# Performance work log

Measured on AMD Instinct MI355X. Metric: run time of the kernel, lower is better.

## Reference

```python
import jax, jax.numpy as jnp
import numpy as np

KS = 2        # kernel_size
DIL = 1       # dilation
FILTERS = 512
Z_DIM = 128
B, C, T = 8, 512, 4096
TZ = T + 2 * (KS - 1)


def _conv1d(x, w, b):
    # x: (B, L, Cin), w: (ks, Cin, Cout) -> VALID conv, channels-last (keras Conv1D)
    y = jax.lax.conv_general_dilated(x, w, window_strides=(1,), padding='VALID',
                                     dimension_numbers=('NWC', 'WIO', 'NWC'))
    return y + b


def _adaptor(z, w1, b1, w2, b2):
    return _conv1d(jax.nn.relu(_conv1d(z, w1, b1)), w2, b2)


def setup_inputs() -> dict:
    key = jax.random.key(0)
    ks = jax.random.split(key, 10)
    lim = np.sqrt(6.0 / FILTERS)
    u = lambda k, shp: jax.random.uniform(k, shp, jnp.float32, -lim, lim)
    return {
        'x': jax.random.normal(ks[0], (B, C, T), jnp.float32),
        'z': jax.random.normal(ks[1], (B, TZ, Z_DIM), jnp.float32),
        'ww1': u(ks[2], (KS, Z_DIM, FILTERS)), 'wb1': jnp.zeros((FILTERS,), jnp.float32),
        'ww2': u(ks[3], (KS, FILTERS, FILTERS)), 'wb2': jnp.zeros((FILTERS,), jnp.float32),
        'bw1': u(ks[4], (KS, Z_DIM, FILTERS)), 'bb1': jnp.zeros((FILTERS,), jnp.float32),
        'bw2': u(ks[5], (KS, FILTERS, FILTERS)), 'bb2': jnp.zeros((FILTERS,), jnp.float32),
    }


def reference(x, z, ww1, wb1, ww2, wb2, bw1, bb1, bw2, bb2):
    m = x.shape[1]
    t = x.shape[2]
    pad = DIL * (KS - 1)
    xp = jnp.pad(x, ((0, 0), (0, 0), (0, pad)))
    end = t + pad
    # im2col-style unfold: (B, C*KS, T)
    xu = jnp.concatenate([xp[:, :, pad - i * DIL: end - i * DIL] for i in range(KS)], axis=1)
    weights = _adaptor(z, ww1, wb1, ww2, wb2)   # (B, T, F)
    bias = _adaptor(z, bw1, bb1, bw2, bb2)      # (B, T, F)
    y = jnp.matmul(xu, weights)                 # (B, C*KS, F)
    return y[:, :m, :] + bias[:, :m, :]
```

## Files before the change

### kernel.cpp

```cpp
#include <hip/hip_runtime.h>

typedef short short8 __attribute__((ext_vector_type(8)));
typedef float float4v __attribute__((ext_vector_type(4)));
typedef __attribute__((address_space(1))) const unsigned int gu32;
typedef __attribute__((address_space(3))) unsigned int lu32;

__device__ __forceinline__ unsigned short f2bf(float f) {
  unsigned int u = __builtin_bit_cast(unsigned int, f);
  u += 0x7FFFu + ((u >> 16) & 1u);
  return (unsigned short)(u >> 16);
}
__device__ __forceinline__ float bf2f(unsigned short s) {
  return __builtin_bit_cast(float, (unsigned int)s << 16);
}

template<int N> __device__ __forceinline__ void vmwait() {
  if constexpr (N == 0) asm volatile("s_waitcnt vmcnt(0)" ::: "memory");
  else if constexpr (N == 2) asm volatile("s_waitcnt vmcnt(2)" ::: "memory");
  else if constexpr (N == 3) asm volatile("s_waitcnt vmcnt(3)" ::: "memory");
  else if constexpr (N == 4) asm volatile("s_waitcnt vmcnt(4)" ::: "memory");
  else if constexpr (N == 6) asm volatile("s_waitcnt vmcnt(6)" ::: "memory");
  else if constexpr (N == 8) asm volatile("s_waitcnt vmcnt(8)" ::: "memory");
}

__global__ __launch_bounds__(256) void prep_w(
    const float* __restrict__ ww1, const float* __restrict__ ww2,
    const float* __restrict__ bw1, const float* __restrict__ bw2,
    const float* __restrict__ z,
    unsigned short* __restrict__ w1T, unsigned short* __restrict__ w2T,
    unsigned short* __restrict__ b1T, unsigned short* __restrict__ b2T,
    unsigned short* __restrict__ zb)
{
  int i = blockIdx.x * 256 + threadIdx.x;
  if (i < 131072) {
    int n = i & 511, k = i >> 9;
    w1T[n * 256 + k] = f2bf(ww1[i]);
  } else if (i < 655360) {
    int j = i - 131072; int n = j & 511, k = j >> 9;
    w2T[n * 1024 + k] = f2bf(ww2[j]);
  } else if (i < 786432) {
    int j = i - 655360; int n = j & 511, k = j >> 9;
    b1T[n * 256 + k] = f2bf(bw1[j]);
  } else if (i < 1310720) {
    int j = i - 786432; int n = j & 511, k = j >> 9;
    b2T[n * 1024 + k] = f2bf(bw2[j]);
  } else {
    int j = i - 1310720;
    zb[j] = f2bf(z[j]);
  }
}

template<int BM, int BN, bool RELU, bool OBF16, bool TRANS, bool SPLITK, int NH,
         bool ROWPACK, bool DBUF>
__device__ __forceinline__ void gemm_core(
    int bx, int by, int bz, int nzTot, unsigned short* smem,
    const unsigned short* __restrict__ A,
    const unsigned short* __restrict__ A2,
    const unsigned short* __restrict__ Bt,
    const float* __restrict__ biasv,
    void* __restrict__ outp,
    void* __restrict__ outp2,
    int M, int Kchunk, int RPB, int EXTRA, int BSCALE,
    int nHalf, int bRowMask,
    long long bStrideB, long long outBatchStride, int outLd)
{
  constexpr int WM = BM / 2, WN = BN / 2;
  constexpr int NI = WM / 16, NJ = WN / 16;
  constexpr int AI = BM / 64;
  constexpr int BI = BN / 64;
  constexpr int SA1 = BM * 32, SB1 = BN * 32;
  unsigned short* sB0 = smem + NH * SA1;

  const int tid  = threadIdx.x;
  const int lane = tid & 63;
  const int wave = tid >> 6;
  const int wm = wave >> 1, wn = wave & 1;
  const int lr = lane & 15, quad = lane >> 4;

  const int r0 = bx * BM;
  const int n0 = by * BN;
  const int bb = r0 / RPB;
  const int Ktot = SPLITK ? Kchunk * nzTot : Kchunk;
  const int kOff = SPLITK ? bz * Kchunk : 0;
  const long long bOffB = (long long)bb * bStrideB;
  const unsigned short* Ae = (nHalf && n0 >= nHalf) ? A2 : A;

  const int srow = lane >> 2;
  const int sg = (lane & 3) ^ (srow & 3);
  const unsigned short* gA[AI];
#pragma unroll
  for (int c = 0; c < AI; ++c) {
    int instr = c * 4 + wave;
    int row = instr * 16 + srow;
    int r = r0 + row; if (r > M - 1) r = M - 1;
    gA[c] = Ae + ((long long)r + (long long)(r / RPB) * EXTRA) * BSCALE + kOff + sg * 8;
  }
  const unsigned short* gB[BI];
#pragma unroll
  for (int c = 0; c < BI; ++c) {
    int instr = c * 4 + wave;
    int row = instr * 16 + srow;
    gB[c] = Bt + (long long)((n0 + row) & bRowMask) * Ktot + bOffB + kOff + sg * 8;
  }

  int aoff[NI], boff[NJ];
#pragma unroll
  for (int i = 0; i < NI; ++i) {
    int rr = wm * WM + i * 16 + lr;
    aoff[i] = rr * 32 + ((quad ^ (rr & 3)) * 8);
  }
#pragma unroll
  for (int j = 0; j < NJ; ++j) {
    int rr = wn * WN + j * 16 + lr;
    boff[j] = rr * 32 + ((quad ^ (rr & 3)) * 8);
  }

  float4v acc[NI][NJ];
  const float4v z4 = {0.f, 0.f, 0.f, 0.f};
#pragma unroll
  for (int i = 0; i < NI; ++i)
#pragma unroll
    for (int j = 0; j < NJ; ++j) acc[i][j] = z4;

  if (DBUF) {
    constexpr int RS = SA1 + SB1;
    const int NT = Kchunk >> 5;
    auto stg = [&](int t, int m) {
      unsigned short* rb = smem + m * RS;
      int kk = t * 32;
#pragma unroll
      for (int c = 0; c < AI; ++c)
        __builtin_amdgcn_global_load_lds((gu32*)(gA[c] + kk),
                                         (lu32*)(rb + (c * 4 + wave) * 512), 16, 0, 0);
#pragma unroll
      for (int c = 0; c < BI; ++c)
        __builtin_amdgcn_global_load_lds((gu32*)(gB[c] + kk),
                                         (lu32*)(rb + SA1 + (c * 4 + wave) * 512), 16, 0, 0);
    };
    stg(0, 0); stg(1, 1);
    int m = 0;
    for (int t = 0; t < NT; ++t) {
      if (t + 1 < NT) vmwait<AI + BI>();
      else            vmwait<0>();
      __builtin_amdgcn_s_barrier();
      __builtin_amdgcn_sched_barrier(0);
      int m2 = m + 2; if (m2 >= 3) m2 -= 3;
      if (t + 2 < NT) stg(t + 2, m2);
      const unsigned short* rb = smem + m * RS;
      short8 af[NI], bfr[NJ];
#pragma unroll
      for (int i = 0; i < NI; ++i) af[i] = *(const short8*)(rb + aoff[i]);
#pragma unroll
      for (int j = 0; j < NJ; ++j) bfr[j] = *(const short8*)(rb + SA1 + boff[j]);
#pragma unroll
      for (int i = 0; i < NI; ++i)
#pragma unroll
        for (int j = 0; j < NJ; ++j)
          acc[i][j] = __builtin_amdgcn_mfma_f32_16x16x32_bf16(af[i], bfr[j], acc[i][j], 0, 0, 0);
      if (++m == 3) m = 0;
    }
    __syncthreads();
  } else {
    for (int k0 = 0; k0 < Kchunk; k0 += 32 * NH) {
#pragma unroll
      for (int h = 0; h < NH; ++h) {
#pragma unroll
        for (int c = 0; c < AI; ++c)
          __builtin_amdgcn_global_load_lds((gu32*)(gA[c] + k0 + h * 32),
                                           (lu32*)(smem + (c * 4 + wave) * 512 + h * SA1), 16, 0, 0);
#pragma unroll
        for (int c = 0; c < BI; ++c)
          __builtin_amdgcn_global_load_lds((gu32*)(gB[c] + k0 + h * 32),
                                           (lu32*)(sB0 + (c * 4 + wave) * 512 + h * SB1), 16, 0, 0);
      }
      __syncthreads();
#pragma unroll
      for (int h = 0; h < NH; ++h) {
        short8 af[NI], bfr[NJ];
#pragma unroll
        for (int i = 0; i < NI; ++i) af[i] = *(const short8*)(smem + h * SA1 + aoff[i]);
#pragma unroll
        for (int j = 0; j < NJ; ++j) bfr[j] = *(const short8*)(sB0 + h * SB1 + boff[j]);
#pragma unroll
        for (int i = 0; i < NI; ++i)
#pragma unroll
          for (int j = 0; j < NJ; ++j)
            acc[i][j] = __builtin_amdgcn_mfma_f32_16x16x32_bf16(af[i], bfr[j], acc[i][j], 0, 0, 0);
      }
      __syncthreads();
    }
  }

  if (TRANS) {
    unsigned short* Ts = smem;
    const int t0l = r0 - bb * RPB;
#pragma unroll
    for (int p = 0; p < 2; ++p) {
      if (wn == p) {
#pragma unroll
        for (int j = 0; j < NJ; ++j) {
          int frl = j * 16 + lr;
          float bv = biasv[n0 + p * WN + frl];
#pragma unroll
          for (int i = 0; i < NI; ++i) {
            int tr = wm * WM + i * 16 + quad * 4;
            unsigned long long pk = 0;
#pragma unroll
            for (int g = 0; g < 4; ++g) {
              float vv = acc[i][j][g] + bv;
              if (RELU) vv = fmaxf(vv, 0.f);
              pk |= (unsigned long long)f2bf(vv) << (16 * g);
            }
            *(unsigned long long*)(Ts + frl * (BM + 8) + tr) = pk;
          }
        }
      }
      __syncthreads();
      int frl = tid >> 2, sgg = tid & 3;
      unsigned short* dst = (unsigned short*)outp + (long long)bb * outBatchStride
                          + (long long)(n0 + p * WN + frl) * outLd + t0l + sgg * (BM / 4);
      const unsigned short* srcp = Ts + frl * (BM + 8) + sgg * (BM / 4);
#pragma unroll
      for (int u = 0; u < BM / 32; ++u)
        *(uint4*)(dst + u * 8) = *(const uint4*)(srcp + u * 8);
      __syncthreads();
    }
  } else if (ROWPACK) {
    constexpr int P  = (BM > 64) ? 2 : 1;
    constexpr int RP = BM / P;
    constexpr int BNP = BN + 8;
    constexpr int TPR = 256 / RP;
    constexpr int EPT = BN / TPR;
    void* op = (SPLITK && bz) ? outp2 : outp;
    unsigned short* R = smem;
#pragma unroll
    for (int p = 0; p < P; ++p) {
      if (P == 1 || wm == p) {
#pragma unroll
        for (int j = 0; j < NJ; ++j) {
          int cc = wn * WN + j * 16 + lr;
#pragma unroll
          for (int i = 0; i < NI; ++i) {
            int rl = (P == 1 ? wm * WM : 0) + i * 16 + quad * 4;
#pragma unroll
            for (int g = 0; g < 4; ++g)
              R[(rl + g) * BNP + cc] = f2bf(acc[i][j][g]);
          }
        }
      }
      __syncthreads();
      int rloc = tid / TPR, part = tid % TPR;
      unsigned short* dstp = (unsigned short*)op
                           + (long long)(r0 + p * RP + rloc) * outLd + n0 + part * EPT;
      const unsigned short* srcp = R + rloc * BNP + part * EPT;
#pragma unroll
      for (int u = 0; u < EPT / 8; ++u)
        *(uint4*)(dstp + u * 8) = *(const uint4*)(srcp + u * 8);
      if (p + 1 < P) __syncthreads();
    }
  } else {
    void* op = (SPLITK && bz) ? outp2 : outp;
#pragma unroll
    for (int j = 0; j < NJ; ++j) {
      int n_g = n0 + wn * WN + j * 16 + lr;
      float bv = biasv ? biasv[n_g] : 0.f;
#pragma unroll
      for (int i = 0; i < NI; ++i) {
        int r_base = r0 + wm * WM + i * 16 + quad * 4;
#pragma unroll
        for (int g = 0; g < 4; ++g) {
          int r_g = r_base + g;
          if (r_g >= M) continue;
          float v = acc[i][j][g] + bv;
          if (RELU) v = fmaxf(v, 0.f);
          long long oidx = (long long)r_g * outLd + n_g;
          if (OBF16) ((unsigned short*)op)[oidx] = f2bf(v);
          else       ((float*)op)[oidx] = v;
        }
      }
    }
  }
}

template<int BM, int BN, bool RELU, bool OBF16, bool TRANS, bool SPLITK, int NH,
         bool ROWPACK, bool DBUF, bool REMAP8>
__global__ __launch_bounds__(256)
void gemm_bt(const unsigned short* __restrict__ A,
             const unsigned short* __restrict__ A2,
             const unsigned short* __restrict__ Bt,
             const float* __restrict__ biasv,
             void* __restrict__ outp,
             void* __restrict__ outp2,
             int M, int Kchunk, int RPB, int EXTRA, int BSCALE,
             int nHalf, int bRowMask,
             long long bStrideB, long long outBatchStride, int outLd)
{
  constexpr int STAGE = DBUF ? 3 * (BM * 32 + BN * 32) : NH * (BM * 32 + BN * 32);
  constexpr int REPK = TRANS ? (BN / 2) * (BM + 8)
                     : (ROWPACK ? (BM > 64 ? (BM / 2) * (BN + 8) : BM * (BN + 8)) : 0);
  constexpr int SMEMN = (REPK > STAGE) ? REPK : STAGE;
  __shared__ unsigned short smem[SMEMN];
  int bx, by, bz, nz;
  if (REMAP8) {
    int lin = blockIdx.x;
    by = lin & 7;
    int pos = lin >> 3;
    bz = pos >> 5;
    bx = pos & 31;
    nz = 2;
  } else {
    bx = blockIdx.x; by = blockIdx.y; bz = blockIdx.z; nz = gridDim.z;
  }
  gemm_core<BM, BN, RELU, OBF16, TRANS, SPLITK, NH, ROWPACK, DBUF>(
      bx, by, bz, nz, smem,
      A, A2, Bt, biasv, outp, outp2,
      M, Kchunk, RPB, EXTRA, BSCALE, nHalf, bRowMask,
      bStrideB, outBatchStride, outLd);
}

__global__ __launch_bounds__(256) void cvt_x(
    const float* __restrict__ x,
    unsigned short* __restrict__ xs,
    unsigned short* __restrict__ xz,
    float* __restrict__ rs)
{
  __shared__ float red[4];
  long long r = blockIdx.x;
  const float* xr = x + r * 4096;
  int t0 = threadIdx.x * 16;
  float v[17];
  const float4* xr4 = (const float4*)(xr + t0);
#pragma unroll
  for (int q = 0; q < 4; ++q) {
    float4 f = xr4[q];
    v[q * 4] = f.x; v[q * 4 + 1] = f.y; v[q * 4 + 2] = f.z; v[q * 4 + 3] = f.w;
  }
  v[16] = (t0 + 16 < 4096) ? xr[t0 + 16] : 0.f;
  unsigned int spk[8], zpk[8];
  float sum = 0.f;
#pragma unroll
  for (int q = 0; q < 8; ++q) {
    unsigned short s0 = f2bf(v[2 * q + 1]);
    unsigned short s1 = f2bf(v[2 * q + 2]);
    sum += bf2f(s0);
    sum += bf2f(s1);
    spk[q] = (unsigned int)s0 | ((unsigned int)s1 << 16);
    unsigned short z0 = (t0 == 0 && q == 0) ? (unsigned short)0 : f2bf(v[2 * q]);
    unsigned short z1 = f2bf(v[2 * q + 1]);
    zpk[q] = (unsigned int)z0 | ((unsigned int)z1 << 16);
  }
  *(uint4*)(xs + r * 4096 + t0)     = *(uint4*)(spk);
  *(uint4*)(xs + r * 4096 + t0 + 8) = *(uint4*)(spk + 4);
  *(uint4*)(xz + r * 4096 + t0)     = *(uint4*)(zpk);
  *(uint4*)(xz + r * 4096 + t0 + 8) = *(uint4*)(zpk + 4);
#pragma unroll
  for (int off = 32; off > 0; off >>= 1) sum += __shfl_down(sum, off);
  if ((threadIdx.x & 63) == 0) red[threadIdx.x >> 6] = sum;
  __syncthreads();
  if (threadIdx.x == 0) rs[r] = red[0] + red[1] + red[2] + red[3];
}

__global__ __launch_bounds__(256) void conv1(
    const unsigned short* __restrict__ zb,
    const unsigned short* __restrict__ w1T,
    const unsigned short* __restrict__ b1T,
    const float* __restrict__ wb1,
    const float* __restrict__ bb1,
    unsigned short* __restrict__ h1T,
    unsigned short* __restrict__ h1b)
{
  __shared__ unsigned short smem[24576];
  int g = blockIdx.x;
  if (g < 1024) {
    gemm_core<128, 128, true, true, true, false, 1, false, true>(
        g & 255, g >> 8, 0, 1, smem,
        zb, nullptr, w1T, wb1, h1T, nullptr,
        32768, 256, 4096, 2, 128, 0, 0xFFFF, 0, 512ll * 4096, 4096);
  } else {
    int idx = g - 1024;
    gemm_core<64, 128, true, true, false, false, 1, false, true>(
        idx % 65, idx / 65, 0, 1, smem,
        zb, nullptr, b1T, bb1, h1b, nullptr,
        4104, 256, 513, 3585, 128, 0, 0xFFFF, 0, 0, 512);
  }
}

__global__ __launch_bounds__(256) void final_gemm3(
    const unsigned short* __restrict__ p0,
    const unsigned short* __restrict__ p1,
    const unsigned short* __restrict__ h1b,
    const unsigned short* __restrict__ w2T,
    const unsigned short* __restrict__ b2T,
    const float* __restrict__ rs,
    const float* __restrict__ wb2,
    const float* __restrict__ bb2,
    float* __restrict__ out)
{
  constexpr int RS = 8192;
  __shared__ unsigned short smem[3 * RS];
  const int tid = threadIdx.x;
  const int lane = tid & 63, wave = tid >> 6;
  const int wm = wave >> 1, wn = wave & 1;
  const int lr = lane & 15, quad = lane >> 4;
  const int r0 = blockIdx.x * 64, n0 = blockIdx.y * 64;

  const int srow = lane >> 2;
  const int sg = (lane & 3) ^ (srow & 3);
  const int row = wave * 16 + srow;
  const int rA = r0 + row;
  const int rB = n0 + row;
  const unsigned short* aP[3] = {
    p0 + (long long)rA * 1024 + sg * 8,
    p1 + (long long)rA * 1024 + sg * 8,
    h1b + ((long long)rA + (rA >> 9)) * 512 + sg * 8 };
  const unsigned short* bP[3] = {
    w2T + (long long)rB * 1024 + sg * 8,
    w2T + (long long)rB * 1024 + sg * 8,
    b2T + (long long)rB * 1024 + sg * 8 };

  int aoff[2], boff[2];
#pragma unroll
  for (int i = 0; i < 2; ++i) {
    int rr = wm * 32 + i * 16 + lr;
    aoff[i] = rr * 32 + ((quad ^ (rr & 3)) * 8);
    int nn = wn * 32 + i * 16 + lr;
    boff[i] = nn * 32 + ((quad ^ (nn & 3)) * 8);
  }

  float4v acc[2][2];
  const float4v z4 = {0.f, 0.f, 0.f, 0.f};
  acc[0][0] = z4; acc[0][1] = z4; acc[1][0] = z4; acc[1][1] = z4;

  const int wslot = wave * 512;
  auto stg = [&](int t, int m) {
    int k = t * 64; int seg = k >> 10; int kk = k & 1023;
    unsigned short* base = smem + m * RS;
    __builtin_amdgcn_global_load_lds((gu32*)(aP[seg] + kk),      (lu32*)(base + wslot), 16, 0, 0);
    __builtin_amdgcn_global_load_lds((gu32*)(aP[seg] + kk + 32), (lu32*)(base + 2048 + wslot), 16, 0, 0);
    __builtin_amdgcn_global_load_lds((gu32*)(bP[seg] + kk),      (lu32*)(base + 4096 + wslot), 16, 0, 0);
    __builtin_amdgcn_global_load_lds((gu32*)(bP[seg] + kk + 32), (lu32*)(base + 6144 + wslot), 16, 0, 0);
  };
  stg(0, 0); stg(1, 1);
  int m = 0;
  for (int t = 0; t < 48; ++t) {
    if (t < 47) vmwait<4>();
    else        vmwait<0>();
    __builtin_amdgcn_s_barrier();
    __builtin_amdgcn_sched_barrier(0);
    int m2 = m + 2; if (m2 >= 3) m2 -= 3;
    if (t + 2 < 48) stg(t + 2, m2);
    const unsigned short* base = smem + m * RS;
#pragma unroll
    for (int h = 0; h < 2; ++h) {
      short8 af[2], bfr[2];
      af[0] = *(const short8*)(base + h * 2048 + aoff[0]);
      af[1] = *(const short8*)(base + h * 2048 + aoff[1]);
      bfr[0] = *(const short8*)(base + 4096 + h * 2048 + boff[0]);
      bfr[1] = *(const short8*)(base + 4096 + h * 2048 + boff[1]);
#pragma unroll
      for (int i = 0; i < 2; ++i)
#pragma unroll
        for (int j = 0; j < 2; ++j)
          acc[i][j] = __builtin_amdgcn_mfma_f32_16x16x32_bf16(af[i], bfr[j], acc[i][j], 0, 0, 0);
    }
    if (++m == 3) m = 0;
  }

#pragma unroll
  for (int j = 0; j < 2; ++j) {
    int n_g = n0 + wn * 32 + j * 16 + lr;
    float w2b = wb2[n_g], bbv = bb2[n_g];
#pragma unroll
    for (int i = 0; i < 2; ++i) {
      int rb2 = r0 + wm * 32 + i * 16 + quad * 4;
#pragma unroll
      for (int g = 0; g < 4; ++g) {
        int r_g = rb2 + g;
        out[(long long)r_g * 512 + n_g] = acc[i][j][g] + rs[r_g] * w2b + bbv;
      }
    }
  }
}

extern "C" void kernel_launch(void* const* d_in, const int* in_sizes, int n_in,
                              void* d_out, int out_size, void* d_ws, size_t ws_size,
                              hipStream_t stream) {
  const float* x   = (const float*)d_in[0];
  const float* z   = (const float*)d_in[1];
  const float* ww1 = (const float*)d_in[2];
  const float* wb1 = (const float*)d_in[3];
  const float* ww2 = (const float*)d_in[4];
  const float* wb2 = (const float*)d_in[5];
  const float* bw1 = (const float*)d_in[6];
  const float* bb1 = (const float*)d_in[7];
  const float* bw2 = (const float*)d_in[8];
  const float* bb2 = (const float*)d_in[9];

  char* ws = (char*)d_ws;
  unsigned short* xs  = (unsigned short*)ws; ws += 16777216ll * 2;
  unsigned short* xz  = (unsigned short*)ws; ws += 16777216ll * 2;
  unsigned short* zb  = (unsigned short*)ws; ws += 4196352ll  * 2;
  unsigned short* h1T = (unsigned short*)ws; ws += 16777216ll * 2;
  unsigned short* h1b = (unsigned short*)ws; ws += 2101248ll  * 2;
  unsigned short* w2T = (unsigned short*)ws; ws += 524288ll * 2;
  unsigned short* b2T = (unsigned short*)ws; ws += 524288ll * 2;
  float* rs = (float*)ws;                    ws += 4096ll * 4;
  char* tail = ws;
  unsigned short* w1T = (unsigned short*)tail;
  unsigned short* b1T = (unsigned short*)tail + 131072;
  unsigned short* p0  = zb;
  unsigned short* p1  = (unsigned short*)tail;

  prep_w<<<21512, 256, 0, stream>>>(ww1, ww2, bw1, bw2, z, w1T, w2T, b1T, b2T, zb);
  cvt_x<<<4096, 256, 0, stream>>>(x, xs, xz, rs);
  conv1<<<1284, 256, 0, stream>>>(zb, w1T, b1T, wb1, bb1, h1T, h1b);
  gemm_bt<128, 128, false, true, false, true, 1, true, true, true><<<512, 256, 0, stream>>>(
      xs, xz, h1T, nullptr, p0, p1,
      4096, 2048, 512, 0, 4096, 512, 511, 512ll * 4096, 0, 1024);
  final_gemm3<<<dim3(64, 8), 256, 0, stream>>>(
      p0, p1, h1b, w2T, b2T, rs, wb2, bb2, (float*)d_out);
}
```

Baseline: 250.7 us.

## Fuse prep kernels, tile weight transpose, deepen LDS pipeline, remap split-K grid

Merges the weight/z conversion and x conversion kernels into one launch, which removes a launch. The weight transpose now goes through an LDS tile so reads and writes are coalesced, and the z conversion is vectorized. The main split-K GEMM and the final GEMM move from a 3-stage to a 4-stage LDS ring with deeper vmcnt waits, to hide more global-load latency at the cost of more shared memory per block. The block-index remap for the split-K GEMM is also changed, which alters tile ordering and cache locality.

```diff
diff --git a/kernel.cpp b/kernel.cpp
--- a/kernel.cpp
+++ b/kernel.cpp
@@ -23,35 +23,93 @@
   else if constexpr (N == 8) asm volatile("s_waitcnt vmcnt(8)" ::: "memory");
 }
 
-__global__ __launch_bounds__(256) void prep_w(
+__global__ __launch_bounds__(256) void prep(
     const float* __restrict__ ww1, const float* __restrict__ ww2,
     const float* __restrict__ bw1, const float* __restrict__ bw2,
-    const float* __restrict__ z,
+    const float* __restrict__ z, const float* __restrict__ x,
     unsigned short* __restrict__ w1T, unsigned short* __restrict__ w2T,
     unsigned short* __restrict__ b1T, unsigned short* __restrict__ b2T,
-    unsigned short* __restrict__ zb)
+    unsigned short* __restrict__ zb,
+    unsigned short* __restrict__ xs, unsigned short* __restrict__ xz,
+    float* __restrict__ rs)
 {
-  int i = blockIdx.x * 256 + threadIdx.x;
-  if (i < 131072) {
-    int n = i & 511, k = i >> 9;
-    w1T[n * 256 + k] = f2bf(ww1[i]);
-  } else if (i < 655360) {
-    int j = i - 131072; int n = j & 511, k = j >> 9;
-    w2T[n * 1024 + k] = f2bf(ww2[j]);
-  } else if (i < 786432) {
-    int j = i - 655360; int n = j & 511, k = j >> 9;
-    b1T[n * 256 + k] = f2bf(bw1[j]);
-  } else if (i < 1310720) {
-    int j = i - 786432; int n = j & 511, k = j >> 9;
-    b2T[n * 1024 + k] = f2bf(bw2[j]);
+  __shared__ float lds[64][65];
+  const int b = blockIdx.x;
+  const int tid = threadIdx.x;
+  if (b < 320) {
+    const float* src; unsigned short* dst; int K, tile;
+    if (b < 32)       { src = ww1; dst = w1T; K = 256;  tile = b; }
+    else if (b < 160) { src = ww2; dst = w2T; K = 1024; tile = b - 32; }
+    else if (b < 192) { src = bw1; dst = b1T; K = 256;  tile = b - 160; }
+    else              { src = bw2; dst = b2T; K = 1024; tile = b - 192; }
+    int ntk = K >> 6;
+    int k0 = (tile % ntk) * 64, n0 = (tile / ntk) * 64;
+    int nl = tid & 63, kh = tid >> 6;
+#pragma unroll
+    for (int p = 0; p < 16; ++p)
+      lds[kh * 16 + p][nl] = src[(long long)(k0 + kh * 16 + p) * 512 + n0 + nl];
+    __syncthreads();
+    int nr = tid >> 2, q = tid & 3;
+    unsigned short tmp[16];
+#pragma unroll
+    for (int u = 0; u < 16; ++u) tmp[u] = f2bf(lds[q * 16 + u][nr]);
+    unsigned short* op = dst + (long long)(n0 + nr) * K + k0 + q * 16;
+    *(uint4*)op = *(uint4*)tmp;
+    *(uint4*)(op + 8) = *(uint4*)(tmp + 8);
+  } else if (b < 1345) {
+    long long base = (long long)(b - 320) * 4096 + tid * 16;
+    if (base < 4196352) {
+      const float4* zp = (const float4*)(z + base);
+      unsigned int pk[8];
+#pragma unroll
+      for (int q2 = 0; q2 < 4; ++q2) {
+        float4 f = zp[q2];
+        pk[q2 * 2]     = (unsigned int)f2bf(f.x) | ((unsigned int)f2bf(f.y) << 16);
+        pk[q2 * 2 + 1] = (unsigned int)f2bf(f.z) | ((unsigned int)f2bf(f.w) << 16);
+      }
+      *(uint4*)(zb + base)     = *(uint4*)pk;
+      *(uint4*)(zb + base + 8) = *(uint4*)(pk + 4);
+    }
   } else {
-    int j = i - 1310720;
-    zb[j] = f2bf(z[j]);
+    float* red = &lds[0][0];
+    long long r = b - 1345;
+    const float* xr = x + r * 4096;
+    int t0 = tid * 16;
+    float v[17];
+    const float4* xr4 = (const float4*)(xr + t0);
+#pragma unroll
+    for (int q = 0; q < 4; ++q) {
+      float4 f = xr4[q];
+      v[q * 4] = f.x; v[q * 4 + 1] = f.y; v[q * 4 + 2] = f.z; v[q * 4 + 3] = f.w;
+    }
+    v[16] = (t0 + 16 < 4096) ? xr[t0 + 16] : 0.f;
+    unsigned int spk[8], zpk[8];
+    float sum = 0.f;
+#pragma unroll
+    for (int q = 0; q < 8; ++q) {
+      unsigned short s0 = f2bf(v[2 * q + 1]);
+      unsigned short s1 = f2bf(v[2 * q + 2]);
+      sum += bf2f(s0);
+      sum += bf2f(s1);
+      spk[q] = (unsigned int)s0 | ((unsigned int)s1 << 16);
+      unsigned short z0 = (t0 == 0 && q == 0) ? (unsigned short)0 : f2bf(v[2 * q]);
+      unsigned short z1 = f2bf(v[2 * q + 1]);
+      zpk[q] = (unsigned int)z0 | ((unsigned int)z1 << 16);
+    }
+    *(uint4*)(xs + r * 4096 + t0)     = *(uint4*)(spk);
+    *(uint4*)(xs + r * 4096 + t0 + 8) = *(uint4*)(spk + 4);
+    *(uint4*)(xz + r * 4096 + t0)     = *(uint4*)(zpk);
+    *(uint4*)(xz + r * 4096 + t0 + 8) = *(uint4*)(zpk + 4);
+#pragma unroll
+    for (int off = 32; off > 0; off >>= 1) sum += __shfl_down(sum, off);
+    if ((tid & 63) == 0) red[tid >> 6] = sum;
+    __syncthreads();
+    if (tid == 0) rs[r] = red[0] + red[1] + red[2] + red[3];
   }
 }
 
 template<int BM, int BN, bool RELU, bool OBF16, bool TRANS, bool SPLITK, int NH,
-         bool ROWPACK, bool DBUF>
+         bool ROWPACK, int NREG>
 __device__ __forceinline__ void gemm_core(
     int bx, int by, int bz, int nzTot, unsigned short* smem,
     const unsigned short* __restrict__ A,
@@ -69,7 +127,7 @@
   constexpr int AI = BM / 64;
   constexpr int BI = BN / 64;
   constexpr int SA1 = BM * 32, SB1 = BN * 32;
-  unsigned short* sB0 = smem + NH * SA1;
+  unsigned short* sB0 = smem + (NREG > 0 ? 1 : NH) * SA1;
 
   const int tid  = threadIdx.x;
   const int lane = tid & 63;
@@ -122,7 +180,7 @@
 #pragma unroll
     for (int j = 0; j < NJ; ++j) acc[i][j] = z4;
 
-  if (DBUF) {
+  if constexpr (NREG > 0) {
     constexpr int RS = SA1 + SB1;
     const int NT = Kchunk >> 5;
     auto stg = [&](int t, int m) {
@@ -137,15 +195,17 @@
         __builtin_amdgcn_global_load_lds((gu32*)(gB[c] + kk),
                                          (lu32*)(rb + SA1 + (c * 4 + wave) * 512), 16, 0, 0);
     };
-    stg(0, 0); stg(1, 1);
+#pragma unroll
+    for (int i = 0; i < NREG - 1; ++i) if (i < NT) stg(i, i);
     int m = 0;
     for (int t = 0; t < NT; ++t) {
-      if (t + 1 < NT) vmwait<AI + BI>();
-      else            vmwait<0>();
+      if (NREG == 4 && t + 3 <= NT) vmwait<2 * (AI + BI)>();
+      else if (t + 2 <= NT)         vmwait<AI + BI>();
+      else                          vmwait<0>();
       __builtin_amdgcn_s_barrier();
       __builtin_amdgcn_sched_barrier(0);
-      int m2 = m + 2; if (m2 >= 3) m2 -= 3;
-      if (t + 2 < NT) stg(t + 2, m2);
+      int m2 = m + NREG - 1; if (m2 >= NREG) m2 -= NREG;
+      if (t + NREG - 1 < NT) stg(t + NREG - 1, m2);
       const unsigned short* rb = smem + m * RS;
       short8 af[NI], bfr[NJ];
 #pragma unroll
@@ -157,7 +217,7 @@
 #pragma unroll
         for (int j = 0; j < NJ; ++j)
           acc[i][j] = __builtin_amdgcn_mfma_f32_16x16x32_bf16(af[i], bfr[j], acc[i][j], 0, 0, 0);
-      if (++m == 3) m = 0;
+      if (++m == NREG) m = 0;
     }
     __syncthreads();
   } else {
@@ -283,7 +343,7 @@
 }
 
 template<int BM, int BN, bool RELU, bool OBF16, bool TRANS, bool SPLITK, int NH,
-         bool ROWPACK, bool DBUF, bool REMAP8>
+         bool ROWPACK, int NREG, bool REMAP>
 __global__ __launch_bounds__(256)
 void gemm_bt(const unsigned short* __restrict__ A,
              const unsigned short* __restrict__ A2,
@@ -295,69 +355,26 @@
              int nHalf, int bRowMask,
              long long bStrideB, long long outBatchStride, int outLd)
 {
-  constexpr int STAGE = DBUF ? 3 * (BM * 32 + BN * 32) : NH * (BM * 32 + BN * 32);
+  constexpr int STAGE = (NREG > 0 ? NREG : NH) * (BM * 32 + BN * 32);
   constexpr int REPK = TRANS ? (BN / 2) * (BM + 8)
                      : (ROWPACK ? (BM > 64 ? (BM / 2) * (BN + 8) : BM * (BN + 8)) : 0);
   constexpr int SMEMN = (REPK > STAGE) ? REPK : STAGE;
   __shared__ unsigned short smem[SMEMN];
   int bx, by, bz, nz;
-  if (REMAP8) {
+  if (REMAP) {
     int lin = blockIdx.x;
-    by = lin & 7;
-    int pos = lin >> 3;
-    bz = pos >> 5;
-    bx = pos & 31;
+    bx = (lin & 7) * 4 + ((lin >> 3) & 3);
+    by = (lin >> 5) & 7;
+    bz = lin >> 8;
     nz = 2;
   } else {
     bx = blockIdx.x; by = blockIdx.y; bz = blockIdx.z; nz = gridDim.z;
   }
-  gemm_core<BM, BN, RELU, OBF16, TRANS, SPLITK, NH, ROWPACK, DBUF>(
+  gemm_core<BM, BN, RELU, OBF16, TRANS, SPLITK, NH, ROWPACK, NREG>(
       bx, by, bz, nz, smem,
       A, A2, Bt, biasv, outp, outp2,
       M, Kchunk, RPB, EXTRA, BSCALE, nHalf, bRowMask,
       bStrideB, outBatchStride, outLd);
-}
-
-__global__ __launch_bounds__(256) void cvt_x(
-    const float* __restrict__ x,
-    unsigned short* __restrict__ xs,
-    unsigned short* __restrict__ xz,
-    float* __restrict__ rs)
-{
-  __shared__ float red[4];
-  long long r = blockIdx.x;
-  const float* xr = x + r * 4096;
-  int t0 = threadIdx.x * 16;
-  float v[17];
-  const float4* xr4 = (const float4*)(xr + t0);
-#pragma unroll
-  for (int q = 0; q < 4; ++q) {
-    float4 f = xr4[q];
-    v[q * 4] = f.x; v[q * 4 + 1] = f.y; v[q * 4 + 2] = f.z; v[q * 4 + 3] = f.w;
-  }
-  v[16] = (t0 + 16 < 4096) ? xr[t0 + 16] : 0.f;
-  unsigned int spk[8], zpk[8];
-  float sum = 0.f;
-#pragma unroll
-  for (int q = 0; q < 8; ++q) {
-    unsigned short s0 = f2bf(v[2 * q + 1]);
-    unsigned short s1 = f2bf(v[2 * q + 2]);
-    sum += bf2f(s0);
-    sum += bf2f(s1);
-    spk[q] = (unsigned int)s0 | ((unsigned int)s1 << 16);
-    unsigned short z0 = (t0 == 0 && q == 0) ? (unsigned short)0 : f2bf(v[2 * q]);
-    unsigned short z1 = f2bf(v[2 * q + 1]);
-    zpk[q] = (unsigned int)z0 | ((unsigned int)z1 << 16);
-  }
-  *(uint4*)(xs + r * 4096 + t0)     = *(uint4*)(spk);
-  *(uint4*)(xs + r * 4096 + t0 + 8) = *(uint4*)(spk + 4);
-  *(uint4*)(xz + r * 4096 + t0)     = *(uint4*)(zpk);
-  *(uint4*)(xz + r * 4096 + t0 + 8) = *(uint4*)(zpk + 4);
-#pragma unroll
-  for (int off = 32; off > 0; off >>= 1) sum += __shfl_down(sum, off);
-  if ((threadIdx.x & 63) == 0) red[threadIdx.x >> 6] = sum;
-  __syncthreads();
-  if (threadIdx.x == 0) rs[r] = red[0] + red[1] + red[2] + red[3];
 }
 
 __global__ __launch_bounds__(256) void conv1(
@@ -372,13 +389,13 @@
   __shared__ unsigned short smem[24576];
   int g = blockIdx.x;
   if (g < 1024) {
-    gemm_core<128, 128, true, true, true, false, 1, false, true>(
+    gemm_core<128, 128, true, true, true, false, 1, false, 3>(
         g & 255, g >> 8, 0, 1, smem,
         zb, nullptr, w1T, wb1, h1T, nullptr,
         32768, 256, 4096, 2, 128, 0, 0xFFFF, 0, 512ll * 4096, 4096);
   } else {
     int idx = g - 1024;
-    gemm_core<64, 128, true, true, false, false, 1, false, true>(
+    gemm_core<64, 128, true, true, false, false, 1, false, 3>(
         idx % 65, idx / 65, 0, 1, smem,
         zb, nullptr, b1T, bb1, h1b, nullptr,
         4104, 256, 513, 3585, 128, 0, 0xFFFF, 0, 0, 512);
@@ -397,7 +414,7 @@
     float* __restrict__ out)
 {
   constexpr int RS = 8192;
-  __shared__ unsigned short smem[3 * RS];
+  __shared__ unsigned short smem[4 * RS];
   const int tid = threadIdx.x;
   const int lane = tid & 63, wave = tid >> 6;
   const int wm = wave >> 1, wn = wave & 1;
@@ -440,15 +457,16 @@
     __builtin_amdgcn_global_load_lds((gu32*)(bP[seg] + kk),      (lu32*)(base + 4096 + wslot), 16, 0, 0);
     __builtin_amdgcn_global_load_lds((gu32*)(bP[seg] + kk + 32), (lu32*)(base + 6144 + wslot), 16, 0, 0);
   };
-  stg(0, 0); stg(1, 1);
+  stg(0, 0); stg(1, 1); stg(2, 2);
   int m = 0;
   for (int t = 0; t < 48; ++t) {
-    if (t < 47) vmwait<4>();
-    else        vmwait<0>();
+    if (t <= 45)      vmwait<8>();
+    else if (t == 46) vmwait<4>();
+    else              vmwait<0>();
     __builtin_amdgcn_s_barrier();
     __builtin_amdgcn_sched_barrier(0);
-    int m2 = m + 2; if (m2 >= 3) m2 -= 3;
-    if (t + 2 < 48) stg(t + 2, m2);
+    int m2 = m + 3; if (m2 >= 4) m2 -= 4;
+    if (t + 3 < 48) stg(t + 3, m2);
     const unsigned short* base = smem + m * RS;
 #pragma unroll
     for (int h = 0; h < 2; ++h) {
@@ -463,7 +481,7 @@
         for (int j = 0; j < 2; ++j)
           acc[i][j] = __builtin_amdgcn_mfma_f32_16x16x32_bf16(af[i], bfr[j], acc[i][j], 0, 0, 0);
     }
-    if (++m == 3) m = 0;
+    if (++m == 4) m = 0;
   }
 
 #pragma unroll
@@ -511,10 +529,10 @@
   unsigned short* p0  = zb;
   unsigned short* p1  = (unsigned short*)tail;
 
-  prep_w<<<21512, 256, 0, stream>>>(ww1, ww2, bw1, bw2, z, w1T, w2T, b1T, b2T, zb);
-  cvt_x<<<4096, 256, 0, stream>>>(x, xs, xz, rs);
+  prep<<<5441, 256, 0, stream>>>(ww1, ww2, bw1, bw2, z, x,
+                                 w1T, w2T, b1T, b2T, zb, xs, xz, rs);
   conv1<<<1284, 256, 0, stream>>>(zb, w1T, b1T, wb1, bb1, h1T, h1b);
-  gemm_bt<128, 128, false, true, false, true, 1, true, true, true><<<512, 256, 0, stream>>>(
+  gemm_bt<128, 128, false, true, false, true, 1, true, 4, true><<<512, 256, 0, stream>>>(
       xs, xz, h1T, nullptr, p0, p1,
       4096, 2048, 512, 0, 4096, 512, 511, 512ll * 4096, 0, 1024);
   final_gemm3<<<dim3(64, 8), 256, 0, stream>>>(
```

New measurement: 232.9 us. 7.1% less time.
